# Kernel tuning notes

Hardware: AMD Instinct MI355X
Metric: run time of the kernel (lower is better)

Reference implementation:

```python
import jax, jax.numpy as jnp
import numpy as np

N = 50000
E = 800000
IN_C, HID_C, OUT_C = 128, 96, 96
EPS = 1e-5


def setup_inputs() -> dict:
    key = jax.random.key(0)
    ks = jax.random.split(key, 16)
    s = lambda k, shape, fan: jax.random.normal(k, shape, jnp.float32) / np.sqrt(fan)
    inp = {
        "x": jax.random.normal(ks[0], (N, IN_C), jnp.float32),
        "edge_index": jax.random.randint(ks[1], (2, E), 0, N, jnp.int64),
        # GCNConv weights (x @ W then aggregate, bias added after)
        "W1": s(ks[2], (IN_C, HID_C), IN_C), "b1": jnp.zeros((HID_C,), jnp.float32),
        "W2": s(ks[3], (HID_C, HID_C), HID_C), "b2": jnp.zeros((HID_C,), jnp.float32),
        "W3": s(ks[4], (HID_C, OUT_C), HID_C), "b3": jnp.zeros((OUT_C,), jnp.float32),
        # BatchNorm affine params
        "g1": jnp.ones((HID_C,), jnp.float32), "bt1": jnp.zeros((HID_C,), jnp.float32),
        "g2": jnp.ones((HID_C,), jnp.float32), "bt2": jnp.zeros((HID_C,), jnp.float32),
        "g3": jnp.ones((OUT_C,), jnp.float32), "bt3": jnp.zeros((OUT_C,), jnp.float32),
        # MLP head
        "fw1": s(ks[5], (OUT_C, 128), OUT_C), "fb1": jnp.zeros((128,), jnp.float32),
        "fw2": s(ks[6], (128, 64), 128), "fb2": jnp.zeros((64,), jnp.float32),
        "fw3": s(ks[7], (64, 32), 64), "fb3": jnp.zeros((32,), jnp.float32),
        "fw4": s(ks[8], (32, 1), 32), "fb4": jnp.zeros((1,), jnp.float32),
    }
    return inp


def gcn_conv(x, W, b, src, dst, n):
    # PyG GCNConv: h = x @ W; add self-loops; sym-normalized scatter-add; + bias
    h = x @ W  # [N, C]
    deg = jax.ops.segment_sum(jnp.ones(src.shape[0], h.dtype), dst, num_segments=n) + 1.0
    dinv = jax.lax.rsqrt(deg)  # deg >= 1 via self-loop
    norm = dinv[src] * dinv[dst]  # [E]
    agg = jax.ops.segment_sum(h[src] * norm[:, None], dst, num_segments=n)
    return agg + h * (dinv * dinv)[:, None] + b  # self-loop term + bias


def batch_norm(x, g, b):
    m = x.mean(axis=0)
    v = x.var(axis=0)  # biased, as torch BN uses in normalization
    return (x - m) * jax.lax.rsqrt(v + EPS) * g + b


def reference(x, edge_index, W1, b1, W2, b2, W3, b3, g1, bt1, g2, bt2, g3, bt3,
              fw1, fb1, fw2, fb2, fw3, fb3, fw4, fb4):
    src, dst = edge_index[0], edge_index[1]
    n = x.shape[0]
    h = jax.nn.relu(batch_norm(gcn_conv(x, W1, b1, src, dst, n), g1, bt1))
    h = jax.nn.relu(batch_norm(gcn_conv(h, W2, b2, src, dst, n), g2, bt2))
    h = jax.nn.relu(batch_norm(gcn_conv(h, W3, b3, src, dst, n), g3, bt3))
    v = h.mean(axis=0)  # graph mean-pool -> [OUT_C]
    v = jax.nn.relu(v @ fw1 + fb1)  # dropout is identity in eval mode
    v = jax.nn.relu(v @ fw2 + fb2)
    v = jax.nn.relu(v @ fw3 + fb3)
    return v @ fw4 + fb4  # [1]
```

## Files before the change

### kernel.cpp

```cpp
#include <hip/hip_runtime.h>
#include <math.h>

#define NCH 96
#define SCAN_TILE 2048

typedef __attribute__((ext_vector_type(8))) short short8;
typedef __attribute__((ext_vector_type(4))) float f32x4;
typedef unsigned short ushort_t;
typedef unsigned int uint_t;

__device__ __forceinline__ uint_t bf16_rne(float f) {
    uint_t u = __builtin_bit_cast(uint_t, f);
    return (u + 0x7FFFu + ((u >> 16) & 1u)) >> 16;
}

__device__ __forceinline__ float4 unp(uint2 u) {
    float4 r;
    r.x = __builtin_bit_cast(float, u.x << 16);
    r.y = __builtin_bit_cast(float, u.x & 0xFFFF0000u);
    r.z = __builtin_bit_cast(float, u.y << 16);
    r.w = __builtin_bit_cast(float, u.y & 0xFFFF0000u);
    return r;
}

__global__ void zero_kernel(int* __restrict__ cnt, float* __restrict__ small,
                            int n, int nsmall) {
    int i = blockIdx.x * blockDim.x + threadIdx.x;
    if (i < n) cnt[i] = 0;
    if (i < nsmall) small[i] = 0.0f;
}

__global__ void count_kernel(const int* __restrict__ dst, int* __restrict__ cnt, int E) {
    int e = blockIdx.x * blockDim.x + threadIdx.x;
    if (e < E) atomicAdd(&cnt[dst[e]], 1);
}

__global__ __launch_bounds__(256) void scanA_kernel(const int* __restrict__ cnt,
                                                    int* __restrict__ bsum, int n) {
    int b = blockIdx.x, t = threadIdx.x;
    int base = b * SCAN_TILE;
    int s = 0;
    for (int i = t; i < SCAN_TILE; i += 256) {
        int idx = base + i;
        if (idx < n) s += cnt[idx];
    }
#pragma unroll
    for (int off = 32; off; off >>= 1) s += __shfl_down(s, off, 64);
    __shared__ int red[4];
    if ((t & 63) == 0) red[t >> 6] = s;
    __syncthreads();
    if (t == 0) bsum[b] = red[0] + red[1] + red[2] + red[3];
}

__global__ __launch_bounds__(256) void scanB_kernel(int* __restrict__ bsum,
                                                    int* __restrict__ rowptrN, int nb) {
    int t = threadIdx.x;
    __shared__ int ps[256];
    int v = (t < nb) ? bsum[t] : 0;
    ps[t] = v;
    __syncthreads();
    for (int off = 1; off < 256; off <<= 1) {
        int add = (t >= off) ? ps[t - off] : 0;
        __syncthreads();
        ps[t] += add;
        __syncthreads();
    }
    if (t < nb) bsum[t] = ps[t] - v;
    if (t == nb - 1) rowptrN[0] = ps[t];
}

__global__ __launch_bounds__(256) void scanC_kernel(int* __restrict__ cnt,
                                                    const int* __restrict__ bsum,
                                                    int* __restrict__ rowptr,
                                                    float* __restrict__ dinv, int n) {
    int b = blockIdx.x, t = threadIdx.x;
    int base = b * SCAN_TILE + t * 8;
    int c[8];
    int s = 0;
#pragma unroll
    for (int j = 0; j < 8; ++j) {
        int idx = base + j;
        c[j] = (idx < n) ? cnt[idx] : 0;
        s += c[j];
    }
    __shared__ int ps[256];
    ps[t] = s;
    __syncthreads();
    for (int off = 1; off < 256; off <<= 1) {
        int add = (t >= off) ? ps[t - off] : 0;
        __syncthreads();
        ps[t] += add;
        __syncthreads();
    }
    int run = bsum[b] + ps[t] - s;
#pragma unroll
    for (int j = 0; j < 8; ++j) {
        int idx = base + j;
        if (idx < n) {
            rowptr[idx] = run;
            cnt[idx] = run;
            dinv[idx] = rsqrtf((float)(c[j] + 1));
            run += c[j];
        }
    }
}

__global__ void fill_kernel(const int* __restrict__ ei, int* __restrict__ fill,
                            int* __restrict__ adj, int E) {
    int e = blockIdx.x * blockDim.x + threadIdx.x;
    if (e < E) {
        int s = ei[e];
        int pos = atomicAdd(&fill[ei[E + e]], 1);
        adj[pos] = s;
    }
}

template <int K, bool BN>
__global__ __launch_bounds__(256) void gemm_mfma(const float* __restrict__ x,
                                                 const float* __restrict__ ab,
                                                 const float* __restrict__ W,
                                                 const float* __restrict__ dinv,
                                                 ushort_t* __restrict__ hs, int n) {
    constexpr int NKS = K / 32;
    constexpr int NFR = NKS * 6 * 512;
    __shared__ short BH[NFR];
    __shared__ short BL[NFR];
    __shared__ float ABl[2 * NCH];

    const int tid = threadIdx.x;
    for (int idx = tid; idx < NFR; idx += 256) {
        int i  = idx & 7;
        int l2 = (idx >> 3) & 63;
        int r  = idx >> 9;
        int ct = r % 6;
        int ks = r / 6;
        int k   = ks * 32 + ((l2 >> 4) << 3) + i;
        int col = ct * 16 + (l2 & 15);
        float w = W[k * NCH + col];
        uint_t hb = bf16_rne(w);
        float hf = __builtin_bit_cast(float, hb << 16);
        uint_t lb = bf16_rne(w - hf);
        BH[idx] = (short)hb;
        BL[idx] = (short)lb;
    }
    if constexpr (BN) {
        if (tid < 2 * NCH) ABl[tid] = ab[tid];
    }
    __syncthreads();

    const int l  = tid & 63;
    const int wv = tid >> 6;
    const int r0 = blockIdx.x * 128 + wv * 32;
    const int klo = (l >> 4) << 3;

    f32x4 acc[2][6] = {};

    for (int ks = 0; ks < NKS; ++ks) {
        float av[8], bv[8];
        if constexpr (BN) {
            int kb = ks * 32 + klo;
#pragma unroll
            for (int i = 0; i < 8; ++i) { av[i] = ABl[kb + i]; bv[i] = ABl[NCH + kb + i]; }
        }
        short8 Ah[2], Al[2];
#pragma unroll
        for (int rt = 0; rt < 2; ++rt) {
            int rg = r0 + rt * 16 + (l & 15);
            rg = rg < n ? rg : n - 1;
            const float* px = x + (size_t)rg * K + ks * 32 + klo;
            float4 f0 = *(const float4*)px;
            float4 f1 = *(const float4*)(px + 4);
            float vv[8] = {f0.x, f0.y, f0.z, f0.w, f1.x, f1.y, f1.z, f1.w};
#pragma unroll
            for (int i = 0; i < 8; ++i) {
                float v = vv[i];
                if constexpr (BN) v = fmaxf(fmaf(v, av[i], bv[i]), 0.0f);
                uint_t hb = bf16_rne(v);
                float hf = __builtin_bit_cast(float, hb << 16);
                uint_t lb = bf16_rne(v - hf);
                Ah[rt][i] = (short)hb;
                Al[rt][i] = (short)lb;
            }
        }
#pragma unroll
        for (int ct = 0; ct < 6; ++ct) {
            int off = ((ks * 6 + ct) << 9) + (l << 3);
            short8 bh = *(const short8*)&BH[off];
            short8 bl = *(const short8*)&BL[off];
#pragma unroll
            for (int rt = 0; rt < 2; ++rt) {
                acc[rt][ct] = __builtin_amdgcn_mfma_f32_16x16x32_bf16(Ah[rt], bh, acc[rt][ct], 0, 0, 0);
                acc[rt][ct] = __builtin_amdgcn_mfma_f32_16x16x32_bf16(Al[rt], bh, acc[rt][ct], 0, 0, 0);
                acc[rt][ct] = __builtin_amdgcn_mfma_f32_16x16x32_bf16(Ah[rt], bl, acc[rt][ct], 0, 0, 0);
            }
        }
    }

#pragma unroll
    for (int rt = 0; rt < 2; ++rt) {
#pragma unroll
        for (int i = 0; i < 4; ++i) {
            int row = r0 + rt * 16 + ((l >> 4) << 2) + i;
            if (row < n) {
                float dv = dinv[row];
#pragma unroll
                for (int ct = 0; ct < 6; ++ct) {
                    float v = acc[rt][ct][i] * dv;
                    hs[(size_t)row * NCH + ct * 16 + (l & 15)] = (ushort_t)bf16_rne(v);
                }
            }
        }
    }
}

__global__ __launch_bounds__(256) void gather_kernel(const int* __restrict__ rowptr,
                                                     const int* __restrict__ adj,
                                                     const float* __restrict__ dinv,
                                                     const ushort_t* __restrict__ HS,
                                                     float* __restrict__ AGG, int n) {
    int wid = (blockIdx.x * 256 + threadIdx.x) >> 6;
    int lane = threadIdx.x & 63;
    if (wid >= n || lane >= 24) return;
    int lo = rowptr[wid], hi = rowptr[wid + 1];
    float dv = dinv[wid];
    const uint_t* HSu = (const uint_t*)HS;
    const int l2 = lane * 2;

    float4 a = unp(*(const uint2*)(HSu + (size_t)wid * 48 + l2));
    float4 b = make_float4(0.f, 0.f, 0.f, 0.f);
    int j = lo;
    for (; j + 1 < hi; j += 2) {
        int s0 = adj[j], s1 = adj[j + 1];
        float4 v0 = unp(*(const uint2*)(HSu + (size_t)s0 * 48 + l2));
        float4 v1 = unp(*(const uint2*)(HSu + (size_t)s1 * 48 + l2));
        a.x += v0.x; a.y += v0.y; a.z += v0.z; a.w += v0.w;
        b.x += v1.x; b.y += v1.y; b.z += v1.z; b.w += v1.w;
    }
    if (j < hi) {
        int s0 = adj[j];
        float4 v0 = unp(*(const uint2*)(HSu + (size_t)s0 * 48 + l2));
        a.x += v0.x; a.y += v0.y; a.z += v0.z; a.w += v0.w;
    }
    a.x = (a.x + b.x) * dv;
    a.y = (a.y + b.y) * dv;
    a.z = (a.z + b.z) * dv;
    a.w = (a.w + b.w) * dv;
    ((float4*)(AGG + (size_t)wid * NCH))[lane] = a;
}

__global__ __launch_bounds__(384) void stats_kernel(const float* __restrict__ t,
                                                    float* __restrict__ sums, int n) {
    int c = threadIdx.x;
    int ry = threadIdx.y;
    float s1 = 0.f, s2 = 0.f;
    for (int r = blockIdx.x * 4 + ry; r < n; r += gridDim.x * 4) {
        float v = t[(size_t)r * NCH + c];
        s1 += v;
        s2 = fmaf(v, v, s2);
    }
    __shared__ float L1[4][NCH], L2[4][NCH];
    L1[ry][c] = s1;
    L2[ry][c] = s2;
    __syncthreads();
    if (ry == 0) {
        s1 = L1[0][c] + L1[1][c] + L1[2][c] + L1[3][c];
        s2 = L2[0][c] + L2[1][c] + L2[2][c] + L2[3][c];
        atomicAdd(&sums[c], s1);
        atomicAdd(&sums[NCH + c], s2);
    }
}

__global__ void bnparam_kernel(const float* __restrict__ sums,
                               const float* __restrict__ g,
                               const float* __restrict__ bt,
                               float* __restrict__ ab, float n) {
    int c = threadIdx.x;
    if (c < NCH) {
        float mean = sums[c] / n;
        float var = sums[NCH + c] / n - mean * mean;
        float a = g[c] * rsqrtf(var + 1e-5f);
        ab[c] = a;
        ab[NCH + c] = bt[c] - mean * a;
    }
}

__global__ __launch_bounds__(384) void apply_pool_kernel(const float* __restrict__ t,
                                                         const float* __restrict__ ab,
                                                         float* __restrict__ pool, int n) {
    int c = threadIdx.x, ry = threadIdx.y;
    float a = ab[c], b = ab[NCH + c];
    float s = 0.f;
    for (int r = blockIdx.x * 4 + ry; r < n; r += gridDim.x * 4) {
        float v = t[(size_t)r * NCH + c];
        s += fmaxf(fmaf(v, a, b), 0.f);
    }
    __shared__ float L[4][NCH];
    L[ry][c] = s;
    __syncthreads();
    if (ry == 0) atomicAdd(&pool[c], L[0][c] + L[1][c] + L[2][c] + L[3][c]);
}

__global__ __launch_bounds__(128) void mlp_kernel(const float* __restrict__ pool,
        const float* __restrict__ fw1, const float* __restrict__ fb1,
        const float* __restrict__ fw2, const float* __restrict__ fb2,
        const float* __restrict__ fw3, const float* __restrict__ fb3,
        const float* __restrict__ fw4, const float* __restrict__ fb4,
        float* __restrict__ out, float invn) {
    __shared__ float v[NCH], l1[128], l2[64], l3[32];
    int t = threadIdx.x;
    if (t < NCH) v[t] = pool[t] * invn;
    __syncthreads();
    {
        float a = fb1[t];
        for (int k = 0; k < NCH; ++k) a = fmaf(v[k], fw1[k * 128 + t], a);
        l1[t] = fmaxf(a, 0.f);
    }
    __syncthreads();
    if (t < 64) {
        float a = fb2[t];
        for (int k = 0; k < 128; ++k) a = fmaf(l1[k], fw2[k * 64 + t], a);
        l2[t] = fmaxf(a, 0.f);
    }
    __syncthreads();
    if (t < 32) {
        float a = fb3[t];
        for (int k = 0; k < 64; ++k) a = fmaf(l2[k], fw3[k * 32 + t], a);
        l3[t] = fmaxf(a, 0.f);
    }
    __syncthreads();
    if (t == 0) {
        float a = fb4[0];
        for (int k = 0; k < 32; ++k) a = fmaf(l3[k], fw4[k], a);
        out[0] = a;
    }
}

extern "C" void kernel_launch(void* const* d_in, const int* in_sizes, int n_in,
                              void* d_out, int out_size, void* d_ws, size_t ws_size,
                              hipStream_t stream) {
    const float* x  = (const float*)d_in[0];
    const int*  ei  = (const int*)d_in[1];
    const float* W1 = (const float*)d_in[2];
    const float* W2 = (const float*)d_in[4];
    const float* W3 = (const float*)d_in[6];
    const float* g1 = (const float*)d_in[8],  *bt1 = (const float*)d_in[9];
    const float* g2 = (const float*)d_in[10], *bt2 = (const float*)d_in[11];
    const float* g3 = (const float*)d_in[12], *bt3 = (const float*)d_in[13];
    const float* fw1 = (const float*)d_in[14], *fb1 = (const float*)d_in[15];
    const float* fw2 = (const float*)d_in[16], *fb2 = (const float*)d_in[17];
    const float* fw3 = (const float*)d_in[18], *fb3 = (const float*)d_in[19];
    const float* fw4 = (const float*)d_in[20], *fb4 = (const float*)d_in[21];
    float* out = (float*)d_out;

    const int N = in_sizes[0] / 128;
    const int E = in_sizes[1] / 2;
    const size_t n96 = (size_t)N * NCH;

    float* ws    = (float*)d_ws;
    float* T     = ws;
    ushort_t* HSB = (ushort_t*)(T + n96);
    float* dinv  = T + n96 + n96 / 2;
    float* sums1 = dinv + N;
    float* sums2 = sums1 + 2 * NCH;
    float* sums3 = sums2 + 2 * NCH;
    float* pool  = sums3 + 2 * NCH;
    float* ab1   = pool + NCH;
    float* ab2   = ab1 + 2 * NCH;
    float* ab3   = ab2 + 2 * NCH;
    int*   cnt   = (int*)(ab3 + 2 * NCH);
    int*   rowptr= cnt + N;
    int*   adj   = rowptr + N + 1;
    int*   bsum  = adj + E;
    const int nsmall = 3 * 2 * NCH + NCH;

    dim3 b96(NCH, 4);
    const int gemmGrid = (N + 127) / 128;
    const int gathGrid = (N + 3) / 4;
    const int nb = (N + SCAN_TILE - 1) / SCAN_TILE;

    zero_kernel<<<(N + 255) / 256, 256, 0, stream>>>(cnt, sums1, N, nsmall);
    count_kernel<<<(E + 255) / 256, 256, 0, stream>>>(ei + E, cnt, E);
    scanA_kernel<<<nb, 256, 0, stream>>>(cnt, bsum, N);
    scanB_kernel<<<1, 256, 0, stream>>>(bsum, rowptr + N, nb);
    scanC_kernel<<<nb, 256, 0, stream>>>(cnt, bsum, rowptr, dinv, N);
    fill_kernel<<<(E + 255) / 256, 256, 0, stream>>>(ei, cnt, adj, E);

    gemm_mfma<128, false><<<gemmGrid, 256, 0, stream>>>(x, nullptr, W1, dinv, HSB, N);
    gather_kernel<<<gathGrid, 256, 0, stream>>>(rowptr, adj, dinv, HSB, T, N);
    stats_kernel<<<512, b96, 0, stream>>>(T, sums1, N);
    bnparam_kernel<<<1, NCH, 0, stream>>>(sums1, g1, bt1, ab1, (float)N);

    gemm_mfma<96, true><<<gemmGrid, 256, 0, stream>>>(T, ab1, W2, dinv, HSB, N);
    gather_kernel<<<gathGrid, 256, 0, stream>>>(rowptr, adj, dinv, HSB, T, N);
    stats_kernel<<<512, b96, 0, stream>>>(T, sums2, N);
    bnparam_kernel<<<1, NCH, 0, stream>>>(sums2, g2, bt2, ab2, (float)N);

    gemm_mfma<96, true><<<gemmGrid, 256, 0, stream>>>(T, ab2, W3, dinv, HSB, N);
    gather_kernel<<<gathGrid, 256, 0, stream>>>(rowptr, adj, dinv, HSB, T, N);
    stats_kernel<<<512, b96, 0, stream>>>(T, sums3, N);
    bnparam_kernel<<<1, NCH, 0, stream>>>(sums3, g3, bt3, ab3, (float)N);

    apply_pool_kernel<<<512, b96, 0, stream>>>(T, ab3, pool, N);
    mlp_kernel<<<1, 128, 0, stream>>>(pool, fw1, fb1, fw2, fb2, fw3, fb3,
                                      fw4, fb4, out, 1.0f / (float)N);
}
```

Baseline: 500.1 us.

## Fuse BN stats into gather, fold BN params into GEMM, bucketed CSR fill

Column statistics for batch norm are now accumulated inside a persistent gather kernel using half-wave (32-lane) node processing, which removes the separate stats pass that re-read T. The bnparam kernels are removed and the BN scale and shift are computed in the GEMM and pool kernel prologues. The CSR fill becomes a two-stage bucketed scatter: edges go into 128-node buckets, then each bucket is placed using shared-memory atomics, which reduces global atomic contention and scattered writes. The weight-fragment staging loop now reads W in coalesced order. Costs are an extra pairs buffer plus an extra pass over the edges, and atomic ordering in the fill is still nondeterministic.

```diff
diff --git a/kernel.cpp b/kernel.cpp
--- a/kernel.cpp
+++ b/kernel.cpp
@@ -69,9 +69,10 @@
     if (t == nb - 1) rowptrN[0] = ps[t];
 }
 
-__global__ __launch_bounds__(256) void scanC_kernel(int* __restrict__ cnt,
+__global__ __launch_bounds__(256) void scanC_kernel(const int* __restrict__ cnt,
                                                     const int* __restrict__ bsum,
                                                     int* __restrict__ rowptr,
+                                                    int* __restrict__ gcur,
                                                     float* __restrict__ dinv, int n) {
     int b = blockIdx.x, t = threadIdx.x;
     int base = b * SCAN_TILE + t * 8;
@@ -98,26 +99,54 @@
         int idx = base + j;
         if (idx < n) {
             rowptr[idx] = run;
-            cnt[idx] = run;
+            if ((idx & 127) == 0) gcur[idx >> 7] = run;
             dinv[idx] = rsqrtf((float)(c[j] + 1));
             run += c[j];
         }
     }
 }
 
-__global__ void fill_kernel(const int* __restrict__ ei, int* __restrict__ fill,
-                            int* __restrict__ adj, int E) {
+__global__ void bscatter_kernel(const int* __restrict__ ei, int* __restrict__ gcur,
+                                int2* __restrict__ pairs, int E) {
     int e = blockIdx.x * blockDim.x + threadIdx.x;
     if (e < E) {
         int s = ei[e];
-        int pos = atomicAdd(&fill[ei[E + e]], 1);
-        adj[pos] = s;
+        int d = ei[E + e];
+        int pos = atomicAdd(&gcur[d >> 7], 1);
+        pairs[pos] = make_int2(s, d);
+    }
+}
+
+__global__ __launch_bounds__(256) void fill2_kernel(const int* __restrict__ rowptr,
+                                                    const int2* __restrict__ pairs,
+                                                    int* __restrict__ adj, int n) {
+    int b = blockIdx.x, t = threadIdx.x;
+    int base = b << 7;
+    __shared__ int lcur[128];
+    if (t < 128) {
+        int nd = base + t;
+        lcur[t] = (nd < n) ? rowptr[nd] : 0;
+    }
+    __shared__ int se, ee;
+    if (t == 0) {
+        se = rowptr[base];
+        int e2 = base + 128; if (e2 > n) e2 = n;
+        ee = rowptr[e2];
+    }
+    __syncthreads();
+    for (int e = se + t; e < ee; e += 256) {
+        int2 p = pairs[e];
+        int pos = atomicAdd(&lcur[p.y & 127], 1);
+        adj[pos] = p.x;
     }
 }
 
 template <int K, bool BN>
 __global__ __launch_bounds__(256) void gemm_mfma(const float* __restrict__ x,
-                                                 const float* __restrict__ ab,
+                                                 const float* __restrict__ sums,
+                                                 const float* __restrict__ g,
+                                                 const float* __restrict__ bt,
+                                                 float fn,
                                                  const float* __restrict__ W,
                                                  const float* __restrict__ dinv,
                                                  ushort_t* __restrict__ hs, int n) {
@@ -128,29 +157,32 @@
     __shared__ float ABl[2 * NCH];
 
     const int tid = threadIdx.x;
-    for (int idx = tid; idx < NFR; idx += 256) {
-        int i  = idx & 7;
-        int l2 = (idx >> 3) & 63;
-        int r  = idx >> 9;
-        int ct = r % 6;
-        int ks = r / 6;
-        int k   = ks * 32 + ((l2 >> 4) << 3) + i;
-        int col = ct * 16 + (l2 & 15);
-        float w = W[k * NCH + col];
-        uint_t hb = bf16_rne(w);
+    for (int w = tid; w < K * NCH; w += 256) {
+        float wv = W[w];
+        int k = w / NCH;
+        int col = w - k * NCH;
+        int ks = k >> 5, kin = k & 31;
+        int idx = ((ks * 6 + (col >> 4)) << 9) + (((kin >> 3) * 16 + (col & 15)) << 3) + (kin & 7);
+        uint_t hb = bf16_rne(wv);
         float hf = __builtin_bit_cast(float, hb << 16);
-        uint_t lb = bf16_rne(w - hf);
+        uint_t lb = bf16_rne(wv - hf);
         BH[idx] = (short)hb;
         BL[idx] = (short)lb;
     }
     if constexpr (BN) {
-        if (tid < 2 * NCH) ABl[tid] = ab[tid];
+        if (tid < NCH) {
+            float mean = sums[tid] / fn;
+            float var = sums[NCH + tid] / fn - mean * mean;
+            float a = g[tid] * rsqrtf(var + 1e-5f);
+            ABl[tid] = a;
+            ABl[NCH + tid] = bt[tid] - mean * a;
+        }
     }
     __syncthreads();
 
     const int l  = tid & 63;
-    const int wv = tid >> 6;
-    const int r0 = blockIdx.x * 128 + wv * 32;
+    const int wv_ = tid >> 6;
+    const int r0 = blockIdx.x * 128 + wv_ * 32;
     const int klo = (l >> 4) << 3;
 
     f32x4 acc[2][6] = {};
@@ -213,82 +245,84 @@
     }
 }
 
-__global__ __launch_bounds__(256) void gather_kernel(const int* __restrict__ rowptr,
-                                                     const int* __restrict__ adj,
-                                                     const float* __restrict__ dinv,
-                                                     const ushort_t* __restrict__ HS,
-                                                     float* __restrict__ AGG, int n) {
-    int wid = (blockIdx.x * 256 + threadIdx.x) >> 6;
-    int lane = threadIdx.x & 63;
-    if (wid >= n || lane >= 24) return;
-    int lo = rowptr[wid], hi = rowptr[wid + 1];
-    float dv = dinv[wid];
+__global__ __launch_bounds__(256) void gather_stats(const int* __restrict__ rowptr,
+                                                    const int* __restrict__ adj,
+                                                    const float* __restrict__ dinv,
+                                                    const ushort_t* __restrict__ HS,
+                                                    float* __restrict__ AGG,
+                                                    float* __restrict__ sums, int n) {
+    const int tid = threadIdx.x;
+    const int hw = tid >> 5;
+    const int lane = tid & 31;
+    const bool act = lane < 24;
     const uint_t* HSu = (const uint_t*)HS;
     const int l2 = lane * 2;
 
-    float4 a = unp(*(const uint2*)(HSu + (size_t)wid * 48 + l2));
-    float4 b = make_float4(0.f, 0.f, 0.f, 0.f);
-    int j = lo;
-    for (; j + 1 < hi; j += 2) {
-        int s0 = adj[j], s1 = adj[j + 1];
-        float4 v0 = unp(*(const uint2*)(HSu + (size_t)s0 * 48 + l2));
-        float4 v1 = unp(*(const uint2*)(HSu + (size_t)s1 * 48 + l2));
-        a.x += v0.x; a.y += v0.y; a.z += v0.z; a.w += v0.w;
-        b.x += v1.x; b.y += v1.y; b.z += v1.z; b.w += v1.w;
-    }
-    if (j < hi) {
-        int s0 = adj[j];
-        float4 v0 = unp(*(const uint2*)(HSu + (size_t)s0 * 48 + l2));
-        a.x += v0.x; a.y += v0.y; a.z += v0.z; a.w += v0.w;
-    }
-    a.x = (a.x + b.x) * dv;
-    a.y = (a.y + b.y) * dv;
-    a.z = (a.z + b.z) * dv;
-    a.w = (a.w + b.w) * dv;
-    ((float4*)(AGG + (size_t)wid * NCH))[lane] = a;
-}
-
-__global__ __launch_bounds__(384) void stats_kernel(const float* __restrict__ t,
-                                                    float* __restrict__ sums, int n) {
-    int c = threadIdx.x;
-    int ry = threadIdx.y;
-    float s1 = 0.f, s2 = 0.f;
-    for (int r = blockIdx.x * 4 + ry; r < n; r += gridDim.x * 4) {
-        float v = t[(size_t)r * NCH + c];
-        s1 += v;
-        s2 = fmaf(v, v, s2);
-    }
-    __shared__ float L1[4][NCH], L2[4][NCH];
-    L1[ry][c] = s1;
-    L2[ry][c] = s2;
-    __syncthreads();
-    if (ry == 0) {
-        s1 = L1[0][c] + L1[1][c] + L1[2][c] + L1[3][c];
-        s2 = L2[0][c] + L2[1][c] + L2[2][c] + L2[3][c];
-        atomicAdd(&sums[c], s1);
-        atomicAdd(&sums[NCH + c], s2);
-    }
-}
-
-__global__ void bnparam_kernel(const float* __restrict__ sums,
-                               const float* __restrict__ g,
-                               const float* __restrict__ bt,
-                               float* __restrict__ ab, float n) {
-    int c = threadIdx.x;
-    if (c < NCH) {
-        float mean = sums[c] / n;
-        float var = sums[NCH + c] / n - mean * mean;
-        float a = g[c] * rsqrtf(var + 1e-5f);
-        ab[c] = a;
-        ab[NCH + c] = bt[c] - mean * a;
+    float4 s1 = make_float4(0.f, 0.f, 0.f, 0.f);
+    float4 s2 = make_float4(0.f, 0.f, 0.f, 0.f);
+
+    for (int node = blockIdx.x * 8 + hw; node < n; node += gridDim.x * 8) {
+        if (act) {
+            int lo = rowptr[node], hi = rowptr[node + 1];
+            float dv = dinv[node];
+            float4 a = unp(*(const uint2*)(HSu + (size_t)node * 48 + l2));
+            float4 b = make_float4(0.f, 0.f, 0.f, 0.f);
+            int j = lo;
+            for (; j + 1 < hi; j += 2) {
+                int s0 = adj[j], s1i = adj[j + 1];
+                float4 v0 = unp(*(const uint2*)(HSu + (size_t)s0 * 48 + l2));
+                float4 v1 = unp(*(const uint2*)(HSu + (size_t)s1i * 48 + l2));
+                a.x += v0.x; a.y += v0.y; a.z += v0.z; a.w += v0.w;
+                b.x += v1.x; b.y += v1.y; b.z += v1.z; b.w += v1.w;
+            }
+            if (j < hi) {
+                int s0 = adj[j];
+                float4 v0 = unp(*(const uint2*)(HSu + (size_t)s0 * 48 + l2));
+                a.x += v0.x; a.y += v0.y; a.z += v0.z; a.w += v0.w;
+            }
+            a.x = (a.x + b.x) * dv;
+            a.y = (a.y + b.y) * dv;
+            a.z = (a.z + b.z) * dv;
+            a.w = (a.w + b.w) * dv;
+            ((float4*)(AGG + (size_t)node * NCH))[lane] = a;
+            s1.x += a.x; s1.y += a.y; s1.z += a.z; s1.w += a.w;
+            s2.x = fmaf(a.x, a.x, s2.x); s2.y = fmaf(a.y, a.y, s2.y);
+            s2.z = fmaf(a.z, a.z, s2.z); s2.w = fmaf(a.w, a.w, s2.w);
+        }
+    }
+
+    __shared__ float R1[8][NCH], R2[8][NCH];
+    if (act) {
+        *(float4*)&R1[hw][lane * 4] = s1;
+        *(float4*)&R2[hw][lane * 4] = s2;
+    }
+    __syncthreads();
+    if (tid < NCH) {
+        float a = 0.f, b = 0.f;
+#pragma unroll
+        for (int h = 0; h < 8; ++h) { a += R1[h][tid]; b += R2[h][tid]; }
+        atomicAdd(&sums[tid], a);
+        atomicAdd(&sums[NCH + tid], b);
     }
 }
 
 __global__ __launch_bounds__(384) void apply_pool_kernel(const float* __restrict__ t,
-                                                         const float* __restrict__ ab,
+                                                         const float* __restrict__ sums,
+                                                         const float* __restrict__ g,
+                                                         const float* __restrict__ bt,
+                                                         float fn,
                                                          float* __restrict__ pool, int n) {
     int c = threadIdx.x, ry = threadIdx.y;
-    float a = ab[c], b = ab[NCH + c];
+    __shared__ float A[NCH], B[NCH];
+    if (ry == 0) {
+        float mean = sums[c] / fn;
+        float var = sums[NCH + c] / fn - mean * mean;
+        float a = g[c] * rsqrtf(var + 1e-5f);
+        A[c] = a;
+        B[c] = bt[c] - mean * a;
+    }
+    __syncthreads();
+    float a = A[c], b = B[c];
     float s = 0.f;
     for (int r = blockIdx.x * 4 + ry; r < n; r += gridDim.x * 4) {
         float v = t[(size_t)r * NCH + c];
@@ -355,6 +389,7 @@
     const int N = in_sizes[0] / 128;
     const int E = in_sizes[1] / 2;
     const size_t n96 = (size_t)N * NCH;
+    const int nbkt = (N + 127) >> 7;
 
     float* ws    = (float*)d_ws;
     float* T     = ws;
@@ -364,43 +399,39 @@
     float* sums2 = sums1 + 2 * NCH;
     float* sums3 = sums2 + 2 * NCH;
     float* pool  = sums3 + 2 * NCH;
-    float* ab1   = pool + NCH;
-    float* ab2   = ab1 + 2 * NCH;
-    float* ab3   = ab2 + 2 * NCH;
-    int*   cnt   = (int*)(ab3 + 2 * NCH);
+    int*   cnt   = (int*)(pool + NCH);
     int*   rowptr= cnt + N;
-    int*   adj   = rowptr + N + 1;
-    int*   bsum  = adj + E;
+    int*   bsum  = rowptr + N + 1;
+    int*   gcur  = bsum + 256;
+    int*   adj   = gcur + nbkt;
+    int2*  pairs = (int2*)(((uintptr_t)(adj + E) + 7) & ~(uintptr_t)7);
     const int nsmall = 3 * 2 * NCH + NCH;
 
     dim3 b96(NCH, 4);
     const int gemmGrid = (N + 127) / 128;
-    const int gathGrid = (N + 3) / 4;
     const int nb = (N + SCAN_TILE - 1) / SCAN_TILE;
 
     zero_kernel<<<(N + 255) / 256, 256, 0, stream>>>(cnt, sums1, N, nsmall);
     count_kernel<<<(E + 255) / 256, 256, 0, stream>>>(ei + E, cnt, E);
     scanA_kernel<<<nb, 256, 0, stream>>>(cnt, bsum, N);
     scanB_kernel<<<1, 256, 0, stream>>>(bsum, rowptr + N, nb);
-    scanC_kernel<<<nb, 256, 0, stream>>>(cnt, bsum, rowptr, dinv, N);
-    fill_kernel<<<(E + 255) / 256, 256, 0, stream>>>(ei, cnt, adj, E);
-
-    gemm_mfma<128, false><<<gemmGrid, 256, 0, stream>>>(x, nullptr, W1, dinv, HSB, N);
-    gather_kernel<<<gathGrid, 256, 0, stream>>>(rowptr, adj, dinv, HSB, T, N);
-    stats_kernel<<<512, b96, 0, stream>>>(T, sums1, N);
-    bnparam_kernel<<<1, NCH, 0, stream>>>(sums1, g1, bt1, ab1, (float)N);
-
-    gemm_mfma<96, true><<<gemmGrid, 256, 0, stream>>>(T, ab1, W2, dinv, HSB, N);
-    gather_kernel<<<gathGrid, 256, 0, stream>>>(rowptr, adj, dinv, HSB, T, N);
-    stats_kernel<<<512, b96, 0, stream>>>(T, sums2, N);
-    bnparam_kernel<<<1, NCH, 0, stream>>>(sums2, g2, bt2, ab2, (float)N);
-
-    gemm_mfma<96, true><<<gemmGrid, 256, 0, stream>>>(T, ab2, W3, dinv, HSB, N);
-    gather_kernel<<<gathGrid, 256, 0, stream>>>(rowptr, adj, dinv, HSB, T, N);
-    stats_kernel<<<512, b96, 0, stream>>>(T, sums3, N);
-    bnparam_kernel<<<1, NCH, 0, stream>>>(sums3, g3, bt3, ab3, (float)N);
-
-    apply_pool_kernel<<<512, b96, 0, stream>>>(T, ab3, pool, N);
+    scanC_kernel<<<nb, 256, 0, stream>>>(cnt, bsum, rowptr, gcur, dinv, N);
+    bscatter_kernel<<<(E + 255) / 256, 256, 0, stream>>>(ei, gcur, pairs, E);
+    fill2_kernel<<<nbkt, 256, 0, stream>>>(rowptr, pairs, adj, N);
+
+    gemm_mfma<128, false><<<gemmGrid, 256, 0, stream>>>(x, nullptr, nullptr, nullptr, 0.f,
+                                                        W1, dinv, HSB, N);
+    gather_stats<<<512, 256, 0, stream>>>(rowptr, adj, dinv, HSB, T, sums1, N);
+
+    gemm_mfma<96, true><<<gemmGrid, 256, 0, stream>>>(T, sums1, g1, bt1, (float)N,
+                                                      W2, dinv, HSB, N);
+    gather_stats<<<512, 256, 0, stream>>>(rowptr, adj, dinv, HSB, T, sums2, N);
+
+    gemm_mfma<96, true><<<gemmGrid, 256, 0, stream>>>(T, sums2, g2, bt2, (float)N,
+                                                      W3, dinv, HSB, N);
+    gather_stats<<<512, 256, 0, stream>>>(rowptr, adj, dinv, HSB, T, sums3, N);
+
+    apply_pool_kernel<<<512, b96, 0, stream>>>(T, sums3, g3, bt3, (float)N, pool, N);
     mlp_kernel<<<1, 128, 0, stream>>>(pool, fw1, fb1, fw2, fb2, fw3, fb3,
                                       fw4, fb4, out, 1.0f / (float)N);
 }
```

Measured after the change: 788.4 us. 57.6% more time.
